# Performance work log

Measured on AMD Instinct MI355X. Metric: run time of the kernel, lower is better.

## Reference

```python
import jax, jax.numpy as jnp
import numpy as np

B, T, IN, H, LAYERS = 32, 512, 512, 512, 2


def _lstm_dir(x, Wx, Wh, b, reverse):
    """AugmentedLstm with highway, one direction.
    x: (B,T,I), Wx: (I,6H), Wh: (H,5H), b: (5H). Returns (B,T,H), h_final, c_final."""
    h = Wh.shape[0]
    # precompute input projections for all timesteps: (T,B,6H)
    px = jnp.einsum('bti,ig->tbg', x, Wx)
    if reverse:
        px = px[::-1]
    bsz = x.shape[0]
    h0 = jnp.zeros((bsz, h), x.dtype)
    c0 = jnp.zeros((bsz, h), x.dtype)

    def step(carry, pxt):
        hp, cp = carry
        ps = hp @ Wh + b  # (B,5H)
        i = jax.nn.sigmoid(pxt[:, 0*h:1*h] + ps[:, 0*h:1*h])
        f = jax.nn.sigmoid(pxt[:, 1*h:2*h] + ps[:, 1*h:2*h])
        g = jnp.tanh(pxt[:, 2*h:3*h] + ps[:, 2*h:3*h])
        o = jax.nn.sigmoid(pxt[:, 3*h:4*h] + ps[:, 3*h:4*h])
        c = i * g + f * cp
        ht = o * jnp.tanh(c)
        # highway: gate*h_t + (1-gate)*(W_x2 x_t)
        r = jax.nn.sigmoid(pxt[:, 4*h:5*h] + ps[:, 4*h:5*h])
        ht = r * ht + (1.0 - r) * pxt[:, 5*h:6*h]
        return (ht, c), ht

    (hf, cf), ys = jax.lax.scan(step, (h0, c0), px)
    if reverse:
        ys = ys[::-1]
    return jnp.transpose(ys, (1, 0, 2)), hf, cf


def setup_inputs() -> dict:
    key = jax.random.key(0)
    ks = jax.random.split(key, 16)
    d = {'x': jax.random.normal(ks[0], (B, T, IN), jnp.float32)}
    in_sizes = [IN, 2 * H]
    i = 1
    for l in range(LAYERS):
        isz = in_sizes[l]
        for dname in ('f', 'b'):
            d[f'Wx{l}{dname}'] = jax.random.normal(ks[i], (isz, 6 * H), jnp.float32) / np.sqrt(isz); i += 1
            d[f'Wh{l}{dname}'] = jax.random.normal(ks[i], (H, 5 * H), jnp.float32) / np.sqrt(H); i += 1
            d[f'b{l}{dname}'] = jnp.zeros((5 * H,), jnp.float32)
    return d


def reference(x, Wx0f, Wh0f, b0f, Wx0b, Wh0b, b0b,
              Wx1f, Wh1f, b1f, Wx1b, Wh1b, b1b):
    params = [((Wx0f, Wh0f, b0f), (Wx0b, Wh0b, b0b)),
              ((Wx1f, Wh1f, b1f), (Wx1b, Wh1b, b1b))]
    out = x
    final_h, final_c = [], []
    for (pf, pb) in params:
        yf, hf, cf = _lstm_dir(out, *pf, reverse=False)
        yb, hb, cb = _lstm_dir(out, *pb, reverse=True)
        out = jnp.concatenate([yf, yb], axis=-1)  # (B,T,2H)
        final_h.append(jnp.concatenate([hf, hb], axis=-1)[None])  # (1,B,2H)
        final_c.append(jnp.concatenate([cf, cb], axis=-1)[None])
    # torch code cats per-layer (1,B,2H) states along dim=1 -> (1, layers*B, 2H)
    final_h = jnp.concatenate(final_h, axis=1)
    final_c = jnp.concatenate(final_c, axis=1)
    return out, final_h, final_c
```

## Files before the change

kernel.cpp:

```cpp
#include <hip/hip_runtime.h>


typedef float f32x4 __attribute__((ext_vector_type(4)));
typedef __bf16 bf16x8 __attribute__((ext_vector_type(8)));
typedef unsigned short us8 __attribute__((ext_vector_type(8)));
typedef unsigned short us4 __attribute__((ext_vector_type(4)));
typedef unsigned int u32x4 __attribute__((ext_vector_type(4)));

__device__ __forceinline__ unsigned short f2bf(float f) {
  unsigned int u = __float_as_uint(f);
  u += 0x7FFFu + ((u >> 16) & 1u);
  return (unsigned short)(u >> 16);
}
__device__ __forceinline__ float bf2f(unsigned int h) {
  return __uint_as_float(h << 16);
}
__device__ __forceinline__ float sigf(float x) { return 1.0f / (1.0f + __expf(-x)); }
__device__ __forceinline__ float tanh_(float x) { return 2.0f / (1.0f + __expf(-2.0f * x)) - 1.0f; }

#define MFMA(a, b, c) __builtin_amdgcn_mfma_f32_16x16x32_bf16((a), (b), (c), 0, 0, 0)
#define GLOAD_LDS(gp, lp)                                                           \
  __builtin_amdgcn_global_load_lds(                                                 \
      (const __attribute__((address_space(1))) void*)(gp),                          \
      (__attribute__((address_space(3))) void*)(lp), 16, 0, 0)

__device__ __forceinline__ void chunk2_ld(const char* p, u32x4& a, u32x4& b) {
  asm volatile("global_load_dwordx4 %0, %2, off sc0 sc1\n\t"
               "global_load_dwordx4 %1, %2, off offset:16 sc0 sc1"
               : "=&v"(a), "=&v"(b) : "v"(p) : "memory");
}
__device__ __forceinline__ void pub16(char* p, u32x4 v) {
  asm volatile("global_store_dwordx4 %0, %1, off sc0 sc1" :: "v"(p), "v"(v) : "memory");
}


__global__ void k_convert_x(const float* __restrict__ x, unsigned short* __restrict__ xb, int n4) {
  int i = blockIdx.x * blockDim.x + threadIdx.x;
  if (i < n4) {
    float4 v = ((const float4*)x)[i];
    us4 o;
    o[0] = f2bf(v.x); o[1] = f2bf(v.y); o[2] = f2bf(v.z); o[3] = f2bf(v.w);
    ((us4*)xb)[i] = o;
  }
}

__global__ __launch_bounds__(256) void k_pack_wxT(
    const float* __restrict__ W0, const float* __restrict__ W1,
    const float* __restrict__ W2, const float* __restrict__ W3,
    unsigned short* __restrict__ o01, unsigned short* __restrict__ o23) {
  int y = blockIdx.z;
  int K = (y >> 1) ? 1024 : 512;
  int kb = blockIdx.y * 32;
  if (kb >= K) return;
  const float* W = (y == 0) ? W0 : (y == 1) ? W1 : (y == 2) ? W2 : W3;
  unsigned short* o = (y >> 1) ? (o23 + (size_t)(y & 1) * 3072 * 1024)
                               : (o01 + (size_t)(y & 1) * 3072 * 512);
  __shared__ float tile[32][33];
  int nb = blockIdx.x * 32;
  int tx = threadIdx.x & 31, ty = threadIdx.x >> 5;
#pragma unroll
  for (int r = 0; r < 4; ++r)
    tile[ty + r * 8][tx] = W[(size_t)(kb + ty + r * 8) * 3072 + nb + tx];
  __syncthreads();
#pragma unroll
  for (int r = 0; r < 4; ++r)
    o[(size_t)(nb + ty + r * 8) * K + kb + tx] = f2bf(tile[tx][ty + r * 8]);
}

__global__ void k_pack_whp(const float* __restrict__ W0, const float* __restrict__ W1,
                           const float* __restrict__ W2, const float* __restrict__ W3,
                           unsigned short* __restrict__ out) {
  int y = blockIdx.y;
  const float* W = (y == 0) ? W0 : (y == 1) ? W1 : (y == 2) ? W2 : W3;
  unsigned short* o = out + (size_t)y * 1310720;
  int v = blockIdx.x * 256 + threadIdx.x;
  int lane = v & 63, ks = (v >> 6) & 15, ns = (v >> 10) & 31, g = v >> 15;
  int col = g * 512 + ns * 16 + (lane & 15);
  int kb = ks * 32 + ((lane >> 4) << 3);
  us8 vec;
#pragma unroll
  for (int e = 0; e < 8; ++e) vec[e] = f2bf(W[(size_t)(kb + e) * 2560 + col]);
  *(us8*)&o[(size_t)v * 8] = vec;
}

__global__ __launch_bounds__(256) void k_gemm(const unsigned short* __restrict__ A,
                                              const unsigned short* __restrict__ BtBase,
                                              unsigned short* __restrict__ CBase, int K) {
  __shared__ __align__(128) unsigned short As[128 * 32];
  __shared__ __align__(128) unsigned short Bs[128 * 32];
  const unsigned short* Bt = BtBase + (size_t)blockIdx.z * 3072 * K;
  unsigned short* C = CBase + (size_t)blockIdx.z * 16384 * 3072;
  int tid = threadIdx.x;
  int w = tid >> 6, l = tid & 63;
  int m0 = blockIdx.x * 128, n0 = blockIdx.y * 128;
  int wr = (w >> 1) * 64, wc = (w & 1) * 64;
  f32x4 acc[4][4];
#pragma unroll
  for (int i = 0; i < 4; ++i)
#pragma unroll
    for (int j = 0; j < 4; ++j) acc[i][j] = (f32x4){0.f, 0.f, 0.f, 0.f};

  for (int k0 = 0; k0 < K; k0 += 32) {
    __syncthreads();
#pragma unroll
    for (int half = 0; half < 2; ++half) {
      int r = w * 32 + half * 16 + (l >> 2);
      int gq = (l & 3) ^ (r & 3);
      GLOAD_LDS(A + (size_t)(m0 + r) * K + k0 + gq * 8, &As[(w * 32 + half * 16) * 32]);
      GLOAD_LDS(Bt + (size_t)(n0 + r) * K + k0 + gq * 8, &Bs[(w * 32 + half * 16) * 32]);
    }
    __syncthreads();
    bf16x8 af[4], bfr[4];
#pragma unroll
    for (int mi = 0; mi < 4; ++mi) {
      int r = wr + mi * 16 + (l & 15);
      int q = (l >> 4) ^ (r & 3);
      af[mi] = __builtin_bit_cast(bf16x8, *(const us8*)&As[r * 32 + q * 8]);
    }
#pragma unroll
    for (int ni = 0; ni < 4; ++ni) {
      int r = wc + ni * 16 + (l & 15);
      int q = (l >> 4) ^ (r & 3);
      bfr[ni] = __builtin_bit_cast(bf16x8, *(const us8*)&Bs[r * 32 + q * 8]);
    }
#pragma unroll
    for (int mi = 0; mi < 4; ++mi)
#pragma unroll
      for (int ni = 0; ni < 4; ++ni) acc[mi][ni] = MFMA(af[mi], bfr[ni], acc[mi][ni]);
  }
#pragma unroll
  for (int mi = 0; mi < 4; ++mi)
#pragma unroll
    for (int ni = 0; ni < 4; ++ni)
#pragma unroll
      for (int r4 = 0; r4 < 4; ++r4) {
        int row = m0 + wr + mi * 16 + (l >> 4) * 4 + r4;
        int rr = ((row & 511) << 5) + (row >> 9);
        int col = n0 + wc + ni * 16 + (l & 15);
        C[(size_t)rr * 3072 + col] = f2bf(acc[mi][ni][r4]);
      }
}

__global__ __launch_bounds__(512, 1) void k_persist(
    const unsigned short* __restrict__ px,
    const unsigned short* __restrict__ wp,
    const float* __restrict__ bias_f, const float* __restrict__ bias_b,
    char* __restrict__ hxc,
    unsigned short* __restrict__ ybf,
    float* __restrict__ yf,
    float* __restrict__ finals,
    int layer) {
  __shared__ float part[2][4][8][160];
  int wg = blockIdx.x;
  int grp = wg >> 4, m = wg & 15;
  int d = grp & 1, q = grp >> 1;
  int tid = threadIdx.x;
  int w = tid >> 6, l = tid & 63;
  int kh = w & 3, nh = w >> 2;
  int ns = m * 2 + nh;
  const unsigned short* wpd = wp + (size_t)d * 1310720;
  const unsigned short* pxd = px + (size_t)d * 16384 * 3072;
  const float* bias = d ? bias_b : bias_f;
  char* hxg = hxc + (size_t)layer * 196608 + (size_t)grp * 12288;

  bf16x8 wf[5][4];
#pragma unroll
  for (int g5 = 0; g5 < 5; ++g5)
#pragma unroll
    for (int kk = 0; kk < 4; ++kk)
      wf[g5][kk] = __builtin_bit_cast(
          bf16x8,
          *(const us8*)&wpd[(size_t)((g5 * 32 + ns) * 16 + (kh * 4 + kk)) * 512 + l * 8]);

  bool epi = tid < 256;
  int r = tid >> 5, j = tid & 31, jg = m * 32 + j, b = q * 8 + r;
  float bv[5];
#pragma unroll
  for (int g5 = 0; g5 < 5; ++g5) bv[g5] = bias[(g5 << 9) + jg];

  float c = 0.f;
  unsigned int xCur[6], xNext[6];
  if (epi) {
    int t0 = d ? 511 : 0;
    const unsigned short* pp = pxd + ((size_t)((t0 << 5) + b)) * 3072 + jg;
#pragma unroll
    for (int q6 = 0; q6 < 6; ++q6) xNext[q6] = pp[q6 << 9];
  }

  bool lrow8 = (l & 15) < 8;
  int row8 = l & 7;
  int sel = l >> 4;
  int p0 = (sel == 1) ? 1 : (sel == 2) ? 2 : (sel == 3) ? 4 : 0;
  bool s1 = (sel == 1), s2 = (sel == 2);
  int coff[4];
#pragma unroll
  for (int kk = 0; kk < 4; ++kk)
    coff[kk] = (((kh * 4 + kk) * 8 + row8) * 6 + p0) * 16;
  int myc = l & 31, pbase = l & 32, prow = 2 * w + (l >> 5);

  for (int s = 0; s < 512; ++s) {
    int t = d ? (511 - s) : s;
    u32x4 ca[4], cb2[4];

    if (s > 0) {
      const char* cb = hxg + (size_t)(s & 1) * 98304;
      unsigned enc = (unsigned)(s | ((~s & 0xFFFF) << 16));
      bool dn[4];
#pragma unroll
      for (int kk = 0; kk < 4; ++kk) dn[kk] = !lrow8;
      long guard = 0;
      bool ok;
      bool first = true;
      do {
        if (!first) __builtin_amdgcn_s_sleep(1);
        first = false;
#pragma unroll
        for (int kk = 0; kk < 4; ++kk)
          if (!dn[kk]) chunk2_ld(cb + coff[kk], ca[kk], cb2[kk]);
        asm volatile("s_waitcnt vmcnt(0)" ::: "memory");
        __builtin_amdgcn_sched_barrier(0);
        bool mine = true;
#pragma unroll
        for (int kk = 0; kk < 4; ++kk) {
          dn[kk] = dn[kk] || ((ca[kk][3] == enc) && (cb2[kk][3] == enc));
          mine = mine && dn[kk];
        }
        ok = (__all((int)mine) != 0);
      } while (!ok && ++guard < 300000L);
    }

    if (epi) {
#pragma unroll
      for (int i = 0; i < 6; ++i) xCur[i] = xNext[i];
      if (s < 511) {
        int tn = d ? (511 - (s + 1)) : (s + 1);
        const unsigned short* pp = pxd + ((size_t)((tn << 5) + b)) * 3072 + jg;
#pragma unroll
        for (int q6 = 0; q6 < 6; ++q6) xNext[q6] = pp[q6 << 9];
      }
    }

    f32x4 acc[5];
#pragma unroll
    for (int g5 = 0; g5 < 5; ++g5) acc[g5] = (f32x4){0.f, 0.f, 0.f, 0.f};
    if (s > 0) {
#pragma unroll
      for (int kk = 0; kk < 4; ++kk) {
        u32x4 a = ca[kk], bb = cb2[kk], f;
        f[0] = s1 ? a[1] : (s2 ? a[2] : a[0]);
        f[1] = s1 ? a[2] : (s2 ? bb[0] : a[1]);
        f[2] = s1 ? bb[0] : (s2 ? bb[1] : a[2]);
        f[3] = s1 ? bb[1] : (s2 ? bb[2] : bb[0]);
        bf16x8 av = __builtin_bit_cast(bf16x8, f);
#pragma unroll
        for (int g5 = 0; g5 < 5; ++g5) acc[g5] = MFMA(av, wf[g5][kk], acc[g5]);
      }
    }
    if (l < 32) {
#pragma unroll
      for (int g5 = 0; g5 < 5; ++g5)
#pragma unroll
        for (int r4 = 0; r4 < 4; ++r4)
          part[s & 1][kh][(l >> 4) * 4 + r4][nh * 80 + g5 * 16 + (l & 15)] = acc[g5][r4];
    }
    __syncthreads();

    if (epi) {
      int cc0 = (j >> 4) * 80 + (j & 15);
      float ps_[5];
#pragma unroll
      for (int g5 = 0; g5 < 5; ++g5) {
        int cc = cc0 + g5 * 16;
        ps_[g5] = part[s & 1][0][r][cc] + part[s & 1][1][r][cc] +
                  part[s & 1][2][r][cc] + part[s & 1][3][r][cc] + bv[g5];
      }
      float x0 = bf2f(xCur[0]), x1 = bf2f(xCur[1]), x2 = bf2f(xCur[2]);
      float x3 = bf2f(xCur[3]), x4 = bf2f(xCur[4]), x5 = bf2f(xCur[5]);
      float iG = sigf(x0 + ps_[0]);
      float fG = sigf(x1 + ps_[1]);
      float gG = tanh_(x2 + ps_[2]);
      float oG = sigf(x3 + ps_[3]);
      float cn = iG * gG + fG * c;
      c = cn;
      float ht = oG * tanh_(cn);
      float rG = sigf(x4 + ps_[4]);
      ht = rG * ht + (1.f - rG) * x5;

      if (s < 511) {
        unsigned int hbits = (unsigned int)f2bf(ht);
        unsigned int vv[6];
#pragma unroll
        for (int i = 0; i < 6; ++i)
          vv[i] = __shfl(hbits, (pbase + myc * 6 + i) & 63);
        unsigned int pw0 = vv[0] | (vv[1] << 16);
        unsigned int pw1 = vv[2] | (vv[3] << 16);
        unsigned int pw2 = vv[4] | (vv[5] << 16);
        if (myc == 5) { pw1 = 0; pw2 = 0; }
        if (myc < 6) {
          char* dst = hxg + (size_t)((s + 1) & 1) * 98304 +
                      (size_t)((m * 8 + prow) * 6 + myc) * 16;
          unsigned enc1 = (unsigned)((s + 1) | ((~(s + 1) & 0xFFFF) << 16));
          u32x4 pv = {pw0, pw1, pw2, enc1};
          pub16(dst, pv);
        }
      }

      size_t yo = ((size_t)(b * 512 + t)) * 1024 + d * 512 + jg;
      if (ybf) ybf[yo] = f2bf(ht);
      else     yf[yo] = ht;
      if (s == 511) {
        int fo = (layer * 32 + b) * 1024 + d * 512 + jg;
        finals[fo] = ht;
        finals[65536 + fo] = cn;
      }
    }
  }
}


extern "C" void kernel_launch(void* const* d_in, const int* in_sizes, int n_in,
                              void* d_out, int out_size, void* d_ws, size_t ws_size,
                              hipStream_t stream) {
  (void)in_sizes; (void)n_in; (void)out_size; (void)ws_size;
  const float* x = (const float*)d_in[0];
  const float* Wx[4] = {(const float*)d_in[1], (const float*)d_in[4],
                        (const float*)d_in[7], (const float*)d_in[10]};
  const float* Wh[4] = {(const float*)d_in[2], (const float*)d_in[5],
                        (const float*)d_in[8], (const float*)d_in[11]};
  const float* bs[4] = {(const float*)d_in[3], (const float*)d_in[6],
                        (const float*)d_in[9], (const float*)d_in[12]};

  char* ws = (char*)d_ws;
  unsigned short* px   = (unsigned short*)(ws);
  unsigned short* whp  = (unsigned short*)(ws + 201326592);
  char*           hxc  = (char*)(ws + 211812352);

  char* ob = (char*)d_out;
  unsigned short* xbf  = (unsigned short*)(ob);
  unsigned short* wxt0 = (unsigned short*)(ob + 16777216);
  unsigned short* wxt1 = (unsigned short*)(ob + 33554432);
  unsigned short* a1bf = (unsigned short*)(ob);
  float* out = (float*)d_out;
  float* finals = out + 16777216;

  k_convert_x<<<8192, 256, 0, stream>>>(x, xbf, 2097152);
  k_pack_wxT<<<dim3(96, 32, 4), 256, 0, stream>>>(Wx[0], Wx[1], Wx[2], Wx[3], wxt0, wxt1);
  k_pack_whp<<<dim3(640, 4), 256, 0, stream>>>(Wh[0], Wh[1], Wh[2], Wh[3], whp);
  hipMemsetAsync(hxc, 0xFF, 393216, stream);

  for (int layer = 0; layer < 2; ++layer) {
    int K = layer ? 1024 : 512;
    const unsigned short* Ag = layer ? a1bf : xbf;
    const unsigned short* wxt = layer ? wxt1 : wxt0;
    k_gemm<<<dim3(128, 24, 2), 256, 0, stream>>>(Ag, wxt, px, K);
    k_persist<<<128, 512, 0, stream>>>(
        px, whp + (size_t)layer * 2621440, bs[layer * 2], bs[layer * 2 + 1],
        hxc, layer ? nullptr : a1bf, layer ? out : nullptr, finals, layer);
  }
}
```

Measured before the change: 3.097 ms.

## Interleave forward and backward LSTM directions within each persistent workgroup

The persistent recurrent kernel now runs both directions in one workgroup, alternating a forward step and a backward step, and launches 64 workgroups instead of 128. The aim is to hide the cross-workgroup spin-wait latency of one direction behind the other direction's compute. The cost is twice the register-resident weights per thread (two 5x4 bf16x8 fragment sets), which risks spills under the 512-thread launch bound. It also halves the number of CUs used, so per-step work on each CU doubles. The single double-buffered partial-sum array is replaced by one single-buffered array per direction, which may add a hazard between a step's epilogue reads and the next step's writes.

Result: slower. 6.188 ms (+99.8%).

```diff
diff --git a/kernel.cpp b/kernel.cpp
--- a/kernel.cpp
+++ b/kernel.cpp
@@ -141,6 +141,135 @@
       }
 }
 
+template <int D>
+__device__ __forceinline__ void lstm_phase(
+    int s, int layer, int m, int w, int l, bool epi,
+    int r, int j, int jg, int b,
+    const bf16x8 (&wf)[5][4], const float (&bv)[5], float& c,
+    unsigned int (&xCur)[6], unsigned int (&xNext)[6],
+    const unsigned short* __restrict__ pxd, char* __restrict__ hxg,
+    const int (&coff)[4], bool lrow8, bool s1, bool s2,
+    int myc, int pbase, int prow,
+    float (&part)[4][8][160],
+    unsigned short* __restrict__ ybf, float* __restrict__ yf,
+    float* __restrict__ finals) {
+  int kh = w & 3, nh = w >> 2;
+  int t = D ? (511 - s) : s;
+  u32x4 ca[4], cb2[4];
+
+  if (s > 0) {
+    const char* cb = hxg + (size_t)(s & 1) * 98304;
+    unsigned enc = (unsigned)(s | ((~s & 0xFFFF) << 16));
+    bool dn[4];
+#pragma unroll
+    for (int kk = 0; kk < 4; ++kk) dn[kk] = !lrow8;
+    long guard = 0;
+    bool ok;
+    bool first = true;
+    do {
+      if (!first) __builtin_amdgcn_s_sleep(1);
+      first = false;
+#pragma unroll
+      for (int kk = 0; kk < 4; ++kk)
+        if (!dn[kk]) chunk2_ld(cb + coff[kk], ca[kk], cb2[kk]);
+      asm volatile("s_waitcnt vmcnt(0)" ::: "memory");
+      __builtin_amdgcn_sched_barrier(0);
+      bool mine = true;
+#pragma unroll
+      for (int kk = 0; kk < 4; ++kk) {
+        dn[kk] = dn[kk] || ((ca[kk][3] == enc) && (cb2[kk][3] == enc));
+        mine = mine && dn[kk];
+      }
+      ok = (__all((int)mine) != 0);
+    } while (!ok && ++guard < 300000L);
+  }
+
+  if (epi) {
+#pragma unroll
+    for (int i = 0; i < 6; ++i) xCur[i] = xNext[i];
+    if (s < 511) {
+      int tn = D ? (511 - (s + 1)) : (s + 1);
+      const unsigned short* pp = pxd + ((size_t)((tn << 5) + b)) * 3072 + jg;
+#pragma unroll
+      for (int q6 = 0; q6 < 6; ++q6) xNext[q6] = pp[q6 << 9];
+    }
+  }
+
+  f32x4 acc[5];
+#pragma unroll
+  for (int g5 = 0; g5 < 5; ++g5) acc[g5] = (f32x4){0.f, 0.f, 0.f, 0.f};
+  if (s > 0) {
+#pragma unroll
+    for (int kk = 0; kk < 4; ++kk) {
+      u32x4 a = ca[kk], bb = cb2[kk], f;
+      f[0] = s1 ? a[1] : (s2 ? a[2] : a[0]);
+      f[1] = s1 ? a[2] : (s2 ? bb[0] : a[1]);
+      f[2] = s1 ? bb[0] : (s2 ? bb[1] : a[2]);
+      f[3] = s1 ? bb[1] : (s2 ? bb[2] : bb[0]);
+      bf16x8 av = __builtin_bit_cast(bf16x8, f);
+#pragma unroll
+      for (int g5 = 0; g5 < 5; ++g5) acc[g5] = MFMA(av, wf[g5][kk], acc[g5]);
+    }
+  }
+  if (l < 32) {
+#pragma unroll
+    for (int g5 = 0; g5 < 5; ++g5)
+#pragma unroll
+      for (int r4 = 0; r4 < 4; ++r4)
+        part[kh][(l >> 4) * 4 + r4][nh * 80 + g5 * 16 + (l & 15)] = acc[g5][r4];
+  }
+  __syncthreads();
+
+  if (epi) {
+    int cc0 = (j >> 4) * 80 + (j & 15);
+    float ps_[5];
+#pragma unroll
+    for (int g5 = 0; g5 < 5; ++g5) {
+      int cc = cc0 + g5 * 16;
+      ps_[g5] = part[0][r][cc] + part[1][r][cc] + part[2][r][cc] + part[3][r][cc] + bv[g5];
+    }
+    float x0 = bf2f(xCur[0]), x1 = bf2f(xCur[1]), x2 = bf2f(xCur[2]);
+    float x3 = bf2f(xCur[3]), x4 = bf2f(xCur[4]), x5 = bf2f(xCur[5]);
+    float iG = sigf(x0 + ps_[0]);
+    float fG = sigf(x1 + ps_[1]);
+    float gG = tanh_(x2 + ps_[2]);
+    float oG = sigf(x3 + ps_[3]);
+    float cn = iG * gG + fG * c;
+    c = cn;
+    float ht = oG * tanh_(cn);
+    float rG = sigf(x4 + ps_[4]);
+    ht = rG * ht + (1.f - rG) * x5;
+
+    if (s < 511) {
+      unsigned int hbits = (unsigned int)f2bf(ht);
+      unsigned int vv[6];
+#pragma unroll
+      for (int i = 0; i < 6; ++i)
+        vv[i] = __shfl(hbits, (pbase + myc * 6 + i) & 63);
+      unsigned int pw0 = vv[0] | (vv[1] << 16);
+      unsigned int pw1 = vv[2] | (vv[3] << 16);
+      unsigned int pw2 = vv[4] | (vv[5] << 16);
+      if (myc == 5) { pw1 = 0; pw2 = 0; }
+      if (myc < 6) {
+        char* dst = hxg + (size_t)((s + 1) & 1) * 98304 +
+                    (size_t)((m * 8 + prow) * 6 + myc) * 16;
+        unsigned enc1 = (unsigned)((s + 1) | ((~(s + 1) & 0xFFFF) << 16));
+        u32x4 pv = {pw0, pw1, pw2, enc1};
+        pub16(dst, pv);
+      }
+    }
+
+    size_t yo = ((size_t)(b * 512 + t)) * 1024 + D * 512 + jg;
+    if (ybf) ybf[yo] = f2bf(ht);
+    else     yf[yo] = ht;
+    if (s == 511) {
+      int fo = (layer * 32 + b) * 1024 + D * 512 + jg;
+      finals[fo] = ht;
+      finals[65536 + fo] = cn;
+    }
+  }
+}
+
 __global__ __launch_bounds__(512, 1) void k_persist(
     const unsigned short* __restrict__ px,
     const unsigned short* __restrict__ wp,
@@ -150,41 +279,45 @@
     float* __restrict__ yf,
     float* __restrict__ finals,
     int layer) {
-  __shared__ float part[2][4][8][160];
+  __shared__ float partF[4][8][160];
+  __shared__ float partB[4][8][160];
   int wg = blockIdx.x;
-  int grp = wg >> 4, m = wg & 15;
-  int d = grp & 1, q = grp >> 1;
+  int q = wg >> 4, m = wg & 15;
   int tid = threadIdx.x;
   int w = tid >> 6, l = tid & 63;
   int kh = w & 3, nh = w >> 2;
   int ns = m * 2 + nh;
-  const unsigned short* wpd = wp + (size_t)d * 1310720;
-  const unsigned short* pxd = px + (size_t)d * 16384 * 3072;
-  const float* bias = d ? bias_b : bias_f;
-  char* hxg = hxc + (size_t)layer * 196608 + (size_t)grp * 12288;
-
-  bf16x8 wf[5][4];
+  const unsigned short* pxdF = px;
+  const unsigned short* pxdB = px + (size_t)16384 * 3072;
+  char* hxgF = hxc + (size_t)layer * 196608 + (size_t)(q * 2 + 0) * 12288;
+  char* hxgB = hxc + (size_t)layer * 196608 + (size_t)(q * 2 + 1) * 12288;
+
+  bf16x8 wfF[5][4], wfB[5][4];
 #pragma unroll
   for (int g5 = 0; g5 < 5; ++g5)
 #pragma unroll
-    for (int kk = 0; kk < 4; ++kk)
-      wf[g5][kk] = __builtin_bit_cast(
-          bf16x8,
-          *(const us8*)&wpd[(size_t)((g5 * 32 + ns) * 16 + (kh * 4 + kk)) * 512 + l * 8]);
+    for (int kk = 0; kk < 4; ++kk) {
+      size_t fo = (size_t)((g5 * 32 + ns) * 16 + (kh * 4 + kk)) * 512 + l * 8;
+      wfF[g5][kk] = __builtin_bit_cast(bf16x8, *(const us8*)&wp[fo]);
+      wfB[g5][kk] = __builtin_bit_cast(bf16x8, *(const us8*)&wp[1310720 + fo]);
+    }
 
   bool epi = tid < 256;
   int r = tid >> 5, j = tid & 31, jg = m * 32 + j, b = q * 8 + r;
-  float bv[5];
-#pragma unroll
-  for (int g5 = 0; g5 < 5; ++g5) bv[g5] = bias[(g5 << 9) + jg];
-
-  float c = 0.f;
-  unsigned int xCur[6], xNext[6];
+  float bvF[5], bvB[5];
+#pragma unroll
+  for (int g5 = 0; g5 < 5; ++g5) {
+    bvF[g5] = bias_f[(g5 << 9) + jg];
+    bvB[g5] = bias_b[(g5 << 9) + jg];
+  }
+
+  float cF = 0.f, cB = 0.f;
+  unsigned int xCurF[6], xNextF[6], xCurB[6], xNextB[6];
   if (epi) {
-    int t0 = d ? 511 : 0;
-    const unsigned short* pp = pxd + ((size_t)((t0 << 5) + b)) * 3072 + jg;
-#pragma unroll
-    for (int q6 = 0; q6 < 6; ++q6) xNext[q6] = pp[q6 << 9];
+    const unsigned short* ppF = pxdF + ((size_t)b) * 3072 + jg;
+    const unsigned short* ppB = pxdB + ((size_t)((511 << 5) + b)) * 3072 + jg;
+#pragma unroll
+    for (int q6 = 0; q6 < 6; ++q6) { xNextF[q6] = ppF[q6 << 9]; xNextB[q6] = ppB[q6 << 9]; }
   }
 
   bool lrow8 = (l & 15) < 8;
@@ -199,121 +332,12 @@
   int myc = l & 31, pbase = l & 32, prow = 2 * w + (l >> 5);
 
   for (int s = 0; s < 512; ++s) {
-    int t = d ? (511 - s) : s;
-    u32x4 ca[4], cb2[4];
-
-    if (s > 0) {
-      const char* cb = hxg + (size_t)(s & 1) * 98304;
-      unsigned enc = (unsigned)(s | ((~s & 0xFFFF) << 16));
-      bool dn[4];
-#pragma unroll
-      for (int kk = 0; kk < 4; ++kk) dn[kk] = !lrow8;
-      long guard = 0;
-      bool ok;
-      bool first = true;
-      do {
-        if (!first) __builtin_amdgcn_s_sleep(1);
-        first = false;
-#pragma unroll
-        for (int kk = 0; kk < 4; ++kk)
-          if (!dn[kk]) chunk2_ld(cb + coff[kk], ca[kk], cb2[kk]);
-        asm volatile("s_waitcnt vmcnt(0)" ::: "memory");
-        __builtin_amdgcn_sched_barrier(0);
-        bool mine = true;
-#pragma unroll
-        for (int kk = 0; kk < 4; ++kk) {
-          dn[kk] = dn[kk] || ((ca[kk][3] == enc) && (cb2[kk][3] == enc));
-          mine = mine && dn[kk];
-        }
-        ok = (__all((int)mine) != 0);
-      } while (!ok && ++guard < 300000L);
-    }
-
-    if (epi) {
-#pragma unroll
-      for (int i = 0; i < 6; ++i) xCur[i] = xNext[i];
-      if (s < 511) {
-        int tn = d ? (511 - (s + 1)) : (s + 1);
-        const unsigned short* pp = pxd + ((size_t)((tn << 5) + b)) * 3072 + jg;
-#pragma unroll
-        for (int q6 = 0; q6 < 6; ++q6) xNext[q6] = pp[q6 << 9];
-      }
-    }
-
-    f32x4 acc[5];
-#pragma unroll
-    for (int g5 = 0; g5 < 5; ++g5) acc[g5] = (f32x4){0.f, 0.f, 0.f, 0.f};
-    if (s > 0) {
-#pragma unroll
-      for (int kk = 0; kk < 4; ++kk) {
-        u32x4 a = ca[kk], bb = cb2[kk], f;
-        f[0] = s1 ? a[1] : (s2 ? a[2] : a[0]);
-        f[1] = s1 ? a[2] : (s2 ? bb[0] : a[1]);
-        f[2] = s1 ? bb[0] : (s2 ? bb[1] : a[2]);
-        f[3] = s1 ? bb[1] : (s2 ? bb[2] : bb[0]);
-        bf16x8 av = __builtin_bit_cast(bf16x8, f);
-#pragma unroll
-        for (int g5 = 0; g5 < 5; ++g5) acc[g5] = MFMA(av, wf[g5][kk], acc[g5]);
-      }
-    }
-    if (l < 32) {
-#pragma unroll
-      for (int g5 = 0; g5 < 5; ++g5)
-#pragma unroll
-        for (int r4 = 0; r4 < 4; ++r4)
-          part[s & 1][kh][(l >> 4) * 4 + r4][nh * 80 + g5 * 16 + (l & 15)] = acc[g5][r4];
-    }
-    __syncthreads();
-
-    if (epi) {
-      int cc0 = (j >> 4) * 80 + (j & 15);
-      float ps_[5];
-#pragma unroll
-      for (int g5 = 0; g5 < 5; ++g5) {
-        int cc = cc0 + g5 * 16;
-        ps_[g5] = part[s & 1][0][r][cc] + part[s & 1][1][r][cc] +
-                  part[s & 1][2][r][cc] + part[s & 1][3][r][cc] + bv[g5];
-      }
-      float x0 = bf2f(xCur[0]), x1 = bf2f(xCur[1]), x2 = bf2f(xCur[2]);
-      float x3 = bf2f(xCur[3]), x4 = bf2f(xCur[4]), x5 = bf2f(xCur[5]);
-      float iG = sigf(x0 + ps_[0]);
-      float fG = sigf(x1 + ps_[1]);
-      float gG = tanh_(x2 + ps_[2]);
-      float oG = sigf(x3 + ps_[3]);
-      float cn = iG * gG + fG * c;
-      c = cn;
-      float ht = oG * tanh_(cn);
-      float rG = sigf(x4 + ps_[4]);
-      ht = rG * ht + (1.f - rG) * x5;
-
-      if (s < 511) {
-        unsigned int hbits = (unsigned int)f2bf(ht);
-        unsigned int vv[6];
-#pragma unroll
-        for (int i = 0; i < 6; ++i)
-          vv[i] = __shfl(hbits, (pbase + myc * 6 + i) & 63);
-        unsigned int pw0 = vv[0] | (vv[1] << 16);
-        unsigned int pw1 = vv[2] | (vv[3] << 16);
-        unsigned int pw2 = vv[4] | (vv[5] << 16);
-        if (myc == 5) { pw1 = 0; pw2 = 0; }
-        if (myc < 6) {
-          char* dst = hxg + (size_t)((s + 1) & 1) * 98304 +
-                      (size_t)((m * 8 + prow) * 6 + myc) * 16;
-          unsigned enc1 = (unsigned)((s + 1) | ((~(s + 1) & 0xFFFF) << 16));
-          u32x4 pv = {pw0, pw1, pw2, enc1};
-          pub16(dst, pv);
-        }
-      }
-
-      size_t yo = ((size_t)(b * 512 + t)) * 1024 + d * 512 + jg;
-      if (ybf) ybf[yo] = f2bf(ht);
-      else     yf[yo] = ht;
-      if (s == 511) {
-        int fo = (layer * 32 + b) * 1024 + d * 512 + jg;
-        finals[fo] = ht;
-        finals[65536 + fo] = cn;
-      }
-    }
+    lstm_phase<0>(s, layer, m, w, l, epi, r, j, jg, b, wfF, bvF, cF,
+                  xCurF, xNextF, pxdF, hxgF, coff, lrow8, s1, s2,
+                  myc, pbase, prow, partF, ybf, yf, finals);
+    lstm_phase<1>(s, layer, m, w, l, epi, r, j, jg, b, wfB, bvB, cB,
+                  xCurB, xNextB, pxdB, hxgB, coff, lrow8, s1, s2,
+                  myc, pbase, prow, partB, ybf, yf, finals);
   }
 }
 
@@ -353,7 +377,7 @@
     const unsigned short* Ag = layer ? a1bf : xbf;
     const unsigned short* wxt = layer ? wxt1 : wxt0;
     k_gemm<<<dim3(128, 24, 2), 256, 0, stream>>>(Ag, wxt, px, K);
-    k_persist<<<128, 512, 0, stream>>>(
+    k_persist<<<64, 512, 0, stream>>>(
         px, whp + (size_t)layer * 2621440, bs[layer * 2], bs[layer * 2 + 1],
         hxc, layer ? nullptr : a1bf, layer ? out : nullptr, finals, layer);
   }
```
